# Kernel tuning notes

Measured on AMD Instinct MI355X. Metric: run time of the kernel, lower is better.

The kernel has to match this reference:

```python
import jax, jax.numpy as jnp
import numpy as np

B, S, D = 4, 2048, 512
H, HD, RL = 8, 64, 64   # nheads, head_dim = D//H, rl_dim
TEMPER = 1.0
BETA = 1.0
SLOPE = 0.01  # LeakyReLU negative slope
LN_EPS = 1e-5


def setup_inputs() -> dict:
    key = jax.random.key(0)
    ks = jax.random.split(key, 12)
    scale = 0.02
    return {
        "h":   jax.random.normal(ks[0], (B, S, D), dtype=jnp.float32),
        "rh":  jax.random.normal(ks[1], (B, S, RL), dtype=jnp.float32),
        "Wl":  jax.random.normal(ks[2], (D, D), dtype=jnp.float32) * scale,   # linear_l (in,out)
        "Wr":  jax.random.normal(ks[3], (D, D), dtype=jnp.float32) * scale,   # linear_r
        "al":  jax.random.normal(ks[4], (HD,), dtype=jnp.float32) * scale,    # att_l: Linear(head_dim,1)
        "ar":  jax.random.normal(ks[5], (HD,), dtype=jnp.float32) * scale,    # att_r
        "Wrs": jax.random.normal(ks[6], (RL, RL * H), dtype=jnp.float32) * scale,  # r_source
        "Wrt": jax.random.normal(ks[7], (RL, RL * H), dtype=jnp.float32) * scale,  # r_target
        "Wf":  jax.random.normal(ks[8], (D, D), dtype=jnp.float32) * scale,   # linear_final
        "ln_g": jnp.ones((D,), dtype=jnp.float32),
        "ln_b": jnp.zeros((D,), dtype=jnp.float32),
    }


def _layer_norm(x, g, b):
    mu = jnp.mean(x, axis=-1, keepdims=True)
    var = jnp.mean(jnp.square(x - mu), axis=-1, keepdims=True)
    return (x - mu) * jax.lax.rsqrt(var + LN_EPS) * g + b


def reference(h, rh, Wl, Wr, al, ar, Wrs, Wrt, Wf, ln_g, ln_b):
    leaky = lambda x: jnp.where(x >= 0, x, SLOPE * x)
    # projections -> [B, H, S, HD]
    fl = (h @ Wl).reshape(B, S, H, HD).transpose(0, 2, 1, 3)
    fr = (h @ Wr).reshape(B, S, H, HD).transpose(0, 2, 1, 3)
    # additive attention logits: [B,H,S,1] + [B,H,1,S]
    sl = jnp.einsum('bhsd,d->bhs', leaky(fl), al)
    sr = jnp.einsum('bhsd,d->bhs', leaky(fr), ar)
    score = sl[:, :, :, None] + sr[:, :, None, :]
    # relation-embedding bilinear bias: r_k @ r_q -> [B,H,S,S]
    r_k = (rh @ Wrs).reshape(B, S, H, RL).transpose(0, 2, 1, 3)   # [B,H,S,RL]
    r_q = (rh @ Wrt).reshape(B, S, H, RL).transpose(0, 2, 3, 1)   # [B,H,RL,S]
    score = score + BETA * jnp.einsum('bhsr,bhrt->bhst', r_k, r_q)
    score = jax.nn.softmax(score / TEMPER, axis=-1)
    # context and output projection (dropout = 0 -> identity)
    context = jnp.einsum('bhst,bhtd->bhsd', score, fr)
    h_sa = context.transpose(0, 2, 1, 3).reshape(B, S, H * HD)
    fh = h_sa @ Wf
    return _layer_norm(h + fh, ln_g, ln_b)
```

## Files before the change

### kernel.cpp

```cpp
#include <hip/hip_runtime.h>
#include <math.h>

#define B_ 4
#define S_ 2048
#define D_ 512
#define H_ 8
#define HD_ 64
#define RL_ 64
#define LN_EPS 1e-5f
#define SLOPE 0.01f
#define LOG2E 1.4426950408889634f

typedef __attribute__((ext_vector_type(8))) __bf16 bf16x8;
typedef __attribute__((ext_vector_type(4))) float f32x4;
typedef __attribute__((ext_vector_type(16))) float f32x16;

__device__ __forceinline__ float leaky(float x) { return x >= 0.f ? x : SLOPE * x; }

__device__ __forceinline__ ushort f2bf(float f) {
    union { float f; unsigned u; } v; v.f = f;
    unsigned r = v.u + 0x7fffu + ((v.u >> 16) & 1u);
    return (ushort)(r >> 16);
}
__device__ __forceinline__ unsigned cvtpk(float a, float b) {
    unsigned r;
    asm("v_cvt_pk_bf16_f32 %0, %1, %2" : "=v"(r) : "v"(a), "v"(b));
    return r;
}

__device__ __forceinline__ void g2lds16(const void* g, void* l) {
    __builtin_amdgcn_global_load_lds(
        (const __attribute__((address_space(1))) void*)(uintptr_t)g,
        (__attribute__((address_space(3))) void*)(uintptr_t)l, 16, 0, 0);
}

__device__ __forceinline__ void plane32swap(unsigned &x, unsigned &y) {
    asm volatile("v_permlane32_swap_b32 %0, %1" : "+v"(x), "+v"(y));
}

__global__ __launch_bounds__(256) void prep(
    const float* __restrict__ h, const float* __restrict__ rh,
    const float* __restrict__ Wr, const float* __restrict__ Wf,
    const float* __restrict__ Wrs, const float* __restrict__ Wrt,
    ushort* __restrict__ hb, ushort* __restrict__ rhb,
    ushort* __restrict__ WrT, ushort* __restrict__ WfT,
    ushort* __restrict__ WrsT, ushort* __restrict__ WrtT)
{
    const int bx = blockIdx.x, tid = threadIdx.x;
    if (bx < 4608) {
        const float* in = (bx < 4096) ? h : rh;
        ushort* o = (bx < 4096) ? hb : rhb;
        const int i = (bx < 4096 ? bx : bx - 4096) * 256 + tid;
        const float4 v = ((const float4*)in)[i];
        ushort4 u; u.x = f2bf(v.x); u.y = f2bf(v.y); u.z = f2bf(v.z); u.w = f2bf(v.w);
        ((ushort4*)o)[i] = u;
        return;
    }
    __shared__ float TS[64][65];
    int t = bx - 4608;
    const float* in; ushort* out; int K, tk, tn;
    if (t < 64)       { in = Wr;  out = WrT;  K = 512; tk = t & 7; tn = t >> 3; }
    else if (t < 128) { in = Wf;  out = WfT;  K = 512; t -= 64; tk = t & 7; tn = t >> 3; }
    else if (t < 136) { in = Wrs; out = WrsT; K = 64;  tk = 0; tn = t - 128; }
    else              { in = Wrt; out = WrtT; K = 64;  tk = 0; tn = t - 136; }
    const int k0 = tk * 64, n0 = tn * 64;
    const int r = tid >> 4, c4 = (tid & 15) * 4;
    #pragma unroll
    for (int p = 0; p < 4; ++p) {
        const int row = r + 16 * p;
        const float4 v = *(const float4*)(in + (size_t)(k0 + row) * 512 + n0 + c4);
        TS[row][c4] = v.x; TS[row][c4 + 1] = v.y;
        TS[row][c4 + 2] = v.z; TS[row][c4 + 3] = v.w;
    }
    __syncthreads();
    #pragma unroll
    for (int p = 0; p < 4; ++p) {
        const int nn = r + 16 * p;
        ushort4 o;
        o.x = f2bf(TS[c4 + 0][nn]); o.y = f2bf(TS[c4 + 1][nn]);
        o.z = f2bf(TS[c4 + 2][nn]); o.w = f2bf(TS[c4 + 3][nn]);
        *(ushort4*)(out + (size_t)(n0 + nn) * K + k0 + c4) = o;
    }
}

__global__ __launch_bounds__(256) void proj(
    const ushort* __restrict__ hb, const ushort* __restrict__ rhb,
    const ushort* __restrict__ WrT, const ushort* __restrict__ WrsT,
    const ushort* __restrict__ WrtT,
    ushort* __restrict__ frT, ushort* __restrict__ rkw, ushort* __restrict__ rqw,
    float* __restrict__ sred, const float* __restrict__ ar)
{
    __shared__ ushort As[2][64 * 32];
    __shared__ ushort Bs[2][128 * 32];

    const int tid = threadIdx.x;
    const int lane = tid & 63, w = tid >> 6;
    const int ln = lane & 15, quad = lane >> 4;
    const int wm = w >> 1, wn = w & 1;
    const int m0 = blockIdx.x * 64, n0 = blockIdx.y * 128;
    const int z = blockIdx.z;

    const ushort* A; const ushort* wt; ushort* co; float scl; int K;
    if (z == 0)      { A = hb;  wt = WrT;  co = frT; scl = LOG2E; K = 512; }
    else if (z == 1) { A = rhb; wt = WrsT; co = rkw; scl = LOG2E; K = 64; }
    else             { A = rhb; wt = WrtT; co = rqw; scl = 1.0f;  K = 64; }

    const int srA = tid >> 2;
    const int lchA = ((lane & 3) - (srA >> 1)) & 3;
    const ushort* AgB = A + (size_t)(m0 + srA) * K + lchA * 8;
    const int srB = w * 32 + (lane >> 2);
    const int lchB = ((lane & 3) - (srB >> 1)) & 3;
    const ushort* BgB0 = wt + (size_t)(n0 + srB) * K + lchB * 8;
    const ushort* BgB1 = BgB0 + (size_t)16 * K;
    const int aoff = tid * 8;
    const int boff = srB * 32 + (lane & 3) * 8;
    const int pc = (quad + (ln >> 1)) & 3;

    g2lds16(AgB, &As[0][aoff]);
    g2lds16(BgB0, &Bs[0][boff]);
    g2lds16(BgB1, &Bs[0][boff + 512]);

    f32x4 acc[2][4] = {};
    int buf = 0;
    for (int k0 = 0; k0 < K; k0 += 32) {
        __syncthreads();
        if (k0 + 32 < K) {
            g2lds16(AgB + k0 + 32, &As[buf ^ 1][aoff]);
            g2lds16(BgB0 + k0 + 32, &Bs[buf ^ 1][boff]);
            g2lds16(BgB1 + k0 + 32, &Bs[buf ^ 1][boff + 512]);
        }
        bf16x8 af[2], bfr[4];
        #pragma unroll
        for (int mi = 0; mi < 2; ++mi)
            af[mi] = *(const bf16x8*)&As[buf][(wm * 32 + mi * 16 + ln) * 32 + pc * 8];
        #pragma unroll
        for (int ni = 0; ni < 4; ++ni)
            bfr[ni] = *(const bf16x8*)&Bs[buf][(wn * 64 + ni * 16 + ln) * 32 + pc * 8];
        #pragma unroll
        for (int mi = 0; mi < 2; ++mi)
            #pragma unroll
            for (int ni = 0; ni < 4; ++ni)
                acc[mi][ni] = __builtin_amdgcn_mfma_f32_16x16x32_bf16(
                    af[mi], bfr[ni], acc[mi][ni], 0, 0, 0);
        buf ^= 1;
    }

    const int head = blockIdx.y * 2 + wn;
    const int b = m0 >> 11;
    const size_t bh = (size_t)b * H_ + head;
    if (z == 0) {
        #pragma unroll
        for (int mi = 0; mi < 2; ++mi) {
            const int s = (m0 & (S_ - 1)) + wm * 32 + mi * 16 + quad * 4;
            const int sp = (s & ~15) | ((((0x1320u >> (quad * 4)) & 0xFu)) << 2);
            #pragma unroll
            for (int ni = 0; ni < 4; ++ni) {
                const int d = ni * 16 + ln;
                ushort4 o;
                o.x = f2bf(acc[mi][ni][0]); o.y = f2bf(acc[mi][ni][1]);
                o.z = f2bf(acc[mi][ni][2]); o.w = f2bf(acc[mi][ni][3]);
                *(ushort4*)(co + (bh * 64 + d) * S_ + sp) = o;
            }
        }
        float a4[4];
        #pragma unroll
        for (int ni = 0; ni < 4; ++ni) a4[ni] = ar[ni * 16 + ln];
        #pragma unroll
        for (int mi = 0; mi < 2; ++mi) {
            const int s = (m0 & (S_ - 1)) + wm * 32 + mi * 16 + quad * 4;
            #pragma unroll
            for (int r = 0; r < 4; ++r) {
                float v = 0.f;
                #pragma unroll
                for (int ni = 0; ni < 4; ++ni)
                    v += leaky(acc[mi][ni][r]) * a4[ni];
                #pragma unroll
                for (int off = 8; off; off >>= 1) v += __shfl_xor(v, off, 16);
                if (ln == 0) sred[bh * S_ + s + r] = v * scl;
            }
        }
    } else {
        #pragma unroll
        for (int mi = 0; mi < 2; ++mi) {
            const int s = (m0 & (S_ - 1)) + wm * 32 + mi * 16 + quad * 4;
            #pragma unroll
            for (int ni = 0; ni < 4; ++ni) {
                const int d = ni * 16 + ln;
                #pragma unroll
                for (int r = 0; r < 4; ++r)
                    co[(bh * S_ + s + r) * 64 + d] = f2bf(acc[mi][ni][r] * scl);
            }
        }
    }
}

#define WAITV(N) asm volatile("s_waitcnt vmcnt(" #N ")" ::: "memory")
#define BARR()   __builtin_amdgcn_s_barrier()

__global__ __launch_bounds__(256, 1) void attn_mfma(
    const ushort* __restrict__ frT, const ushort* __restrict__ rk,
    const ushort* __restrict__ rq, const float* __restrict__ sr,
    ushort* __restrict__ hsa)
{
    __shared__ ushort SMEM[16384];
    __shared__ float  LS[4][2][64];
    ushort* RQp = SMEM;
    ushort* FTp = SMEM + 8192;

    const int tid = threadIdx.x;
    const int w = tid >> 6;
    const int qg = w >> 1;
    const int th = w & 1;
    const int lane = tid & 63;
    const int lq = lane & 31;
    const int hi = lane >> 5;

    const int flat = blockIdx.x + 16 * (blockIdx.y + 8 * blockIdx.z);
    const int wid = (flat & 7) * 64 + (flat >> 3);
    const int q0 = (wid & 15) * 128;
    const int h = (wid >> 4) & 7;
    const int b = wid >> 7;
    const size_t bh = (size_t)b * H_ + h;
    const int qb = q0 + 64 * qg;

    bf16x8 bq[2][4];
    #pragma unroll
    for (int qt = 0; qt < 2; ++qt) {
        const ushort* p = rk + ((bh * S_ + qb + 32 * qt + lq) << 6) + hi * 8;
        #pragma unroll
        for (int ks = 0; ks < 4; ++ks)
            bq[qt][ks] = *(const bf16x8*)(p + ks * 16);
    }

    const ushort* rq_g = rq + (bh * S_ << 6);
    const ushort* ft_g = frT + (size_t)bh * 64 * S_;
    const float* srp = sr + bh * S_;

    const int srow = tid >> 3;
    const int pg = tid & 7;
    const int oS = (pg - (srow & 7)) & 7;

    #define STAGE(BUF, t0)                                                    \
        { _Pragma("unroll")                                                   \
          for (int j = 0; j < 2; ++j) {                                       \
            const int rr = 32 * j + srow;                                     \
            g2lds16(rq_g + ((size_t)((t0) + rr) << 6) + oS * 8,               \
                    RQp + (BUF) * 4096 + rr * 64 + pg * 8);                   \
            g2lds16(ft_g + (size_t)rr * S_ + (t0) + oS * 8,                   \
                    FTp + (BUF) * 4096 + rr * 64 + pg * 8);                   \
          } }

    f32x16 ctx[2][2] = {};
    float lsum[2] = {0.f, 0.f};

    #define COMPUTE(BI, TC)                                                    \
    {                                                                          \
        bf16x8 af[4];                                                          \
        _Pragma("unroll")                                                      \
        for (int ks = 0; ks < 4; ++ks)                                         \
            af[ks] = *(const bf16x8*)(RQp + (BI) * 4096 + (th * 32 + lq) * 64  \
                       + ((2 * ks + hi + (lq & 7)) & 7) * 8);                  \
        f32x16 s0 = {}; f32x16 s1 = {};                                        \
        _Pragma("unroll")                                                      \
        for (int ks = 0; ks < 4; ++ks) {                                       \
            s0 = __builtin_amdgcn_mfma_f32_32x32x16_bf16(af[ks], bq[0][ks], s0, 0, 0, 0); \
            s1 = __builtin_amdgcn_mfma_f32_32x32x16_bf16(af[ks], bq[1][ks], s1, 0, 0, 0); \
        }                                                                      \
        float sva[16];                                                         \
        _Pragma("unroll")                                                      \
        for (int jj = 0; jj < 4; ++jj) {                                       \
            const float4 v = *(const float4*)(srp + (TC) + th * 32 + jj * 8 + hi * 4); \
            sva[jj * 4 + 0] = v.x; sva[jj * 4 + 1] = v.y;                      \
            sva[jj * 4 + 2] = v.z; sva[jj * 4 + 3] = v.w;                      \
        }                                                                      \
        uint4 paw[2][2];                                                       \
        _Pragma("unroll")                                                      \
        for (int qt = 0; qt < 2; ++qt) {                                       \
            float p[16];                                                       \
            _Pragma("unroll")                                                  \
            for (int r = 0; r < 16; ++r)                                       \
                p[r] = __builtin_amdgcn_exp2f((qt ? s1[r] : s0[r]) + sva[r]);  \
            float ls = 0.f;                                                    \
            _Pragma("unroll")                                                  \
            for (int r = 0; r < 16; ++r) ls += p[r];                           \
            lsum[qt] += ls;                                                    \
            _Pragma("unroll")                                                  \
            for (int c = 0; c < 2; ++c) {                                      \
                const int e = 8 * c;                                           \
                unsigned c01 = cvtpk(p[e + 0], p[e + 1]);                      \
                unsigned c23 = cvtpk(p[e + 2], p[e + 3]);                      \
                unsigned c45 = cvtpk(p[e + 4], p[e + 5]);                      \
                unsigned c67 = cvtpk(p[e + 6], p[e + 7]);                      \
                plane32swap(c45, c67);                                         \
                paw[qt][c] = make_uint4(c01, c23, c67, c45);                   \
            }                                                                  \
        }                                                                      \
        _Pragma("unroll")                                                      \
        for (int c = 0; c < 2; ++c) {                                          \
            _Pragma("unroll")                                                  \
            for (int dt = 0; dt < 2; ++dt) {                                   \
                const bf16x8 fv = *(const bf16x8*)(FTp + (BI) * 4096           \
                    + (dt * 32 + lq) * 64                                      \
                    + ((4 * th + 2 * c + hi + (lq & 7)) & 7) * 8);             \
                ctx[0][dt] = __builtin_amdgcn_mfma_f32_32x32x16_bf16(          \
                    __builtin_bit_cast(bf16x8, paw[0][c]), fv, ctx[0][dt], 0, 0, 0); \
                ctx[1][dt] = __builtin_amdgcn_mfma_f32_32x32x16_bf16(          \
                    __builtin_bit_cast(bf16x8, paw[1][c]), fv, ctx[1][dt], 0, 0, 0); \
            }                                                                  \
        }                                                                      \
    }

    STAGE(0, 0)
    for (int it = 0; it < 15; ++it) {
        const int t0 = it * 128;
        WAITV(0); BARR();
        STAGE(1, t0 + 64)
        COMPUTE(0, t0)
        WAITV(0); BARR();
        STAGE(0, t0 + 128)
        COMPUTE(1, t0 + 64)
    }
    WAITV(0); BARR();
    STAGE(1, 1984)
    COMPUTE(0, 1920)
    WAITV(0); BARR();
    COMPUTE(1, 1984)

    BARR();
    float* CX = (float*)SMEM;
    float* CXw = CX + w * 2048;

    #define EPILOGUE(OWN, OTH)                                                \
    {                                                                         \
        _Pragma("unroll")                                                     \
        for (int qt = 0; qt < 2; ++qt)                                        \
            _Pragma("unroll")                                                 \
            for (int r = 0; r < 16; ++r)                                      \
                CXw[(qt * 16 + r) * 64 + lane] = ctx[qt][OTH][r];             \
        LS[w][0][lane] = lsum[0];                                             \
        LS[w][1][lane] = lsum[1];                                             \
        BARR();                                                               \
        const float* CXp = CX + (w ^ 1) * 2048;                               \
        _Pragma("unroll")                                                     \
        for (int qt = 0; qt < 2; ++qt) {                                      \
            float lt = lsum[qt] + LS[w ^ 1][qt][lane];                        \
            const float l = lt + __shfl_xor(lt, 32, 64);                      \
            const float inv = 1.f / l;                                        \
            _Pragma("unroll")                                                 \
            for (int r = 0; r < 16; ++r) {                                    \
                const float cv = ctx[qt][OWN][r] + CXp[(qt * 16 + r) * 64 + lane]; \
                const int rho = (r & 3) + 8 * (r >> 2) + 4 * hi;              \
                const float fi = __shfl(inv, rho, 64);                        \
                const int q = qb + 32 * qt + rho;                             \
                hsa[(size_t)(b * S_ + q) * D_ + h * 64 + (OWN) * 32 + lq] = f2bf(cv * fi); \
            }                                                                 \
        }                                                                     \
    }

    if (th == 0) EPILOGUE(0, 1)
    else         EPILOGUE(1, 0)
}

__global__ __launch_bounds__(256, 1) void gemm_ln(
    const ushort* __restrict__ A, const ushort* __restrict__ WT,
    const float* __restrict__ hres, const float* __restrict__ g,
    const float* __restrict__ bb, float* __restrict__ out)
{
    __shared__ ushort As[2][32 * 32];
    __shared__ ushort Bs[2][512 * 32];
    __shared__ float  RS[32][4];

    const int tid = threadIdx.x;
    const int lane = tid & 63, w = tid >> 6;
    const int ln = lane & 15, quad = lane >> 4;
    const int K = 512;

    const int blk = (blockIdx.x & 7) * 32 + (blockIdx.x >> 3);
    const int m0 = blk * 32;

    const int srA = tid >> 2;
    const int lchA = ((lane & 3) - (srA >> 1)) & 3;
    const ushort* AgB = A + (size_t)(m0 + srA) * K + lchA * 8;
    const int aoff = tid * 8;

    const int rb = 128 * w + (lane >> 2);

    f32x4 acc[2][8] = {};

    if (tid < 128) g2lds16(AgB, &As[0][aoff]);
    #pragma unroll
    for (int j = 0; j < 8; ++j) {
        const int rw = rb + 16 * j;
        const int lchB = ((lane & 3) - (rw >> 1)) & 3;
        g2lds16(WT + (size_t)rw * K + lchB * 8, &Bs[0][rw * 32 + (lane & 3) * 8]);
    }

    const int pc = (quad + (ln >> 1)) & 3;
    int buf = 0;
    for (int k0 = 0; k0 < K; k0 += 32) {
        __syncthreads();
        if (k0 + 32 < K) {
            if (tid < 128) g2lds16(AgB + k0 + 32, &As[buf ^ 1][aoff]);
            #pragma unroll
            for (int j = 0; j < 8; ++j) {
                const int rw = rb + 16 * j;
                const int lchB = ((lane & 3) - (rw >> 1)) & 3;
                g2lds16(WT + (size_t)rw * K + k0 + 32 + lchB * 8,
                        &Bs[buf ^ 1][rw * 32 + (lane & 3) * 8]);
            }
        }
        bf16x8 af[2], bfr[8];
        #pragma unroll
        for (int mi = 0; mi < 2; ++mi)
            af[mi] = *(const bf16x8*)&As[buf][(mi * 16 + ln) * 32 + pc * 8];
        #pragma unroll
        for (int ni = 0; ni < 8; ++ni)
            bfr[ni] = *(const bf16x8*)&Bs[buf][(w * 128 + ni * 16 + ln) * 32 + pc * 8];
        #pragma unroll
        for (int mi = 0; mi < 2; ++mi)
            #pragma unroll
            for (int ni = 0; ni < 8; ++ni)
                acc[mi][ni] = __builtin_amdgcn_mfma_f32_16x16x32_bf16(
                    af[mi], bfr[ni], acc[mi][ni], 0, 0, 0);
        buf ^= 1;
    }

    float gg[8], bv[8];
    #pragma unroll
    for (int ni = 0; ni < 8; ++ni) {
        const int col = 128 * w + ni * 16 + ln;
        gg[ni] = g[col]; bv[ni] = bb[col];
    }

    #pragma unroll
    for (int mi = 0; mi < 2; ++mi)
        #pragma unroll
        for (int r = 0; r < 4; ++r) {
            const int rl = mi * 16 + quad * 4 + r;
            const float* hp = hres + (size_t)(m0 + rl) * 512 + 128 * w + ln;
            float s = 0.f;
            #pragma unroll
            for (int ni = 0; ni < 8; ++ni) {
                acc[mi][ni][r] += hp[ni * 16];
                s += acc[mi][ni][r];
            }
            #pragma unroll
            for (int off = 8; off; off >>= 1) s += __shfl_xor(s, off, 16);
            if (ln == 0) RS[rl][w] = s;
        }
    __syncthreads();
    float mu[2][4];
    #pragma unroll
    for (int mi = 0; mi < 2; ++mi)
        #pragma unroll
        for (int r = 0; r < 4; ++r) {
            const int rl = mi * 16 + quad * 4 + r;
            mu[mi][r] = (RS[rl][0] + RS[rl][1] + RS[rl][2] + RS[rl][3]) * (1.f / 512.f);
        }
    __syncthreads();
    #pragma unroll
    for (int mi = 0; mi < 2; ++mi)
        #pragma unroll
        for (int r = 0; r < 4; ++r) {
            const int rl = mi * 16 + quad * 4 + r;
            float v = 0.f;
            #pragma unroll
            for (int ni = 0; ni < 8; ++ni) {
                const float d = acc[mi][ni][r] - mu[mi][r];
                v += d * d;
            }
            #pragma unroll
            for (int off = 8; off; off >>= 1) v += __shfl_xor(v, off, 16);
            if (ln == 0) RS[rl][w] = v;
        }
    __syncthreads();
    #pragma unroll
    for (int mi = 0; mi < 2; ++mi)
        #pragma unroll
        for (int r = 0; r < 4; ++r) {
            const int rl = mi * 16 + quad * 4 + r;
            const float var = (RS[rl][0] + RS[rl][1] + RS[rl][2] + RS[rl][3]) * (1.f / 512.f);
            const float inv = rsqrtf(var + LN_EPS);
            float* op = out + (size_t)(m0 + rl) * 512 + 128 * w + ln;
            #pragma unroll
            for (int ni = 0; ni < 8; ++ni)
                op[ni * 16] = (acc[mi][ni][r] - mu[mi][r]) * inv * gg[ni] + bv[ni];
        }
}

extern "C" void kernel_launch(void* const* d_in, const int* in_sizes, int n_in,
                              void* d_out, int out_size, void* d_ws, size_t ws_size,
                              hipStream_t stream)
{
    const float* h   = (const float*)d_in[0];
    const float* rh  = (const float*)d_in[1];
    const float* Wr  = (const float*)d_in[3];
    const float* ar  = (const float*)d_in[5];
    const float* Wrs = (const float*)d_in[6];
    const float* Wrt = (const float*)d_in[7];
    const float* Wf  = (const float*)d_in[8];
    const float* lng = (const float*)d_in[9];
    const float* lnb = (const float*)d_in[10];
    float* out = (float*)d_out;
    char* wsb  = (char*)d_ws;

    const size_t MB = (size_t)1 << 20;
    ushort* hb   = (ushort*)(wsb);
    ushort* rhb  = (ushort*)(wsb + 8 * MB);
    ushort* WrT  = (ushort*)(wsb + 9 * MB);
    ushort* WfT  = (ushort*)(wsb + 9 * MB + 512 * 1024);
    ushort* WrsT = (ushort*)(wsb + 10 * MB);
    ushort* WrtT = (ushort*)(wsb + 10 * MB + 64 * 1024);
    ushort* frT  = (ushort*)(wsb + 11 * MB);
    ushort* rkw  = (ushort*)(wsb + 19 * MB);
    ushort* rqw  = (ushort*)(wsb + 27 * MB);
    float*  sr   = (float*) (wsb + 35 * MB);
    ushort* hsab = (ushort*)(wsb + 36 * MB);

    dim3 blk(256);
    prep<<<dim3(4752), blk, 0, stream>>>(h, rh, Wr, Wf, Wrs, Wrt,
                                         hb, rhb, WrT, WfT, WrsT, WrtT);
    proj<<<dim3(128, 4, 3), blk, 0, stream>>>(hb, rhb, WrT, WrsT, WrtT,
                                              frT, rkw, rqw, sr, ar);
    attn_mfma<<<dim3(S_ / 128, H_, B_), blk, 0, stream>>>(frT, rkw, rqw, sr, hsab);
    gemm_ln<<<dim3(256), blk, 0, stream>>>(hsab, WfT, h, lng, lnb, out);
}
```

Measured before the change: 177.7 us.

## Stage proj outputs through LDS for coalesced stores; halve gemm_ln row tile

The proj kernel's non-score branch now writes its bf16 results into shared memory first, then stores them back to global memory as contiguous 16-byte rows instead of scattered 2-byte writes. The final GEMM+LayerNorm kernel drops from 32-row to 16-row tiles and launches 512 blocks instead of 256, so more CUs have work on the 256-CU-class device. In exchange, each gemm_ln block reads the full Wf tile for half as many rows, which doubles weight traffic. The projection epilogue also gains extra barriers.

```diff
diff --git a/kernel.cpp b/kernel.cpp
--- a/kernel.cpp
+++ b/kernel.cpp
@@ -180,16 +180,33 @@
             }
         }
     } else {
+        __syncthreads();
+        ushort* TMP = &Bs[0][0];
         #pragma unroll
         for (int mi = 0; mi < 2; ++mi) {
-            const int s = (m0 & (S_ - 1)) + wm * 32 + mi * 16 + quad * 4;
+            const int sl = wm * 32 + mi * 16 + quad * 4;
             #pragma unroll
             for (int ni = 0; ni < 4; ++ni) {
-                const int d = ni * 16 + ln;
+                const int c = wn * 64 + ni * 16 + ln;
                 #pragma unroll
                 for (int r = 0; r < 4; ++r)
-                    co[(bh * S_ + s + r) * 64 + d] = f2bf(acc[mi][ni][r] * scl);
+                    TMP[(sl + r) * 128 + c] = f2bf(acc[mi][ni][r] * scl);
             }
+        }
+        __syncthreads();
+        const int rr = tid >> 4;
+        const int cc = (tid & 15) * 8;
+        const int hh = cc >> 6;
+        const size_t bhb = (size_t)b * H_ + blockIdx.y * 2 + hh;
+        #pragma unroll
+        for (int p = 0; p < 4; ++p) {
+            const int row = rr + 16 * p;
+            const int s = (m0 & (S_ - 1)) + row;
+            const ushort4 v0 = *(const ushort4*)&TMP[row * 128 + cc];
+            const ushort4 v1 = *(const ushort4*)&TMP[row * 128 + cc + 4];
+            ushort* dst = co + (bhb * S_ + s) * 64 + (cc & 63);
+            *(ushort4*)dst = v0;
+            *(ushort4*)(dst + 4) = v1;
         }
     }
 }
@@ -366,17 +383,17 @@
     const float* __restrict__ hres, const float* __restrict__ g,
     const float* __restrict__ bb, float* __restrict__ out)
 {
-    __shared__ ushort As[2][32 * 32];
+    __shared__ ushort As[2][16 * 32];
     __shared__ ushort Bs[2][512 * 32];
-    __shared__ float  RS[32][4];
+    __shared__ float  RS[16][4];
 
     const int tid = threadIdx.x;
     const int lane = tid & 63, w = tid >> 6;
     const int ln = lane & 15, quad = lane >> 4;
     const int K = 512;
 
-    const int blk = (blockIdx.x & 7) * 32 + (blockIdx.x >> 3);
-    const int m0 = blk * 32;
+    const int blk = (blockIdx.x & 7) * 64 + (blockIdx.x >> 3);
+    const int m0 = blk * 16;
 
     const int srA = tid >> 2;
     const int lchA = ((lane & 3) - (srA >> 1)) & 3;
@@ -385,9 +402,9 @@
 
     const int rb = 128 * w + (lane >> 2);
 
-    f32x4 acc[2][8] = {};
-
-    if (tid < 128) g2lds16(AgB, &As[0][aoff]);
+    f32x4 acc[8] = {};
+
+    if (tid < 64) g2lds16(AgB, &As[0][aoff]);
     #pragma unroll
     for (int j = 0; j < 8; ++j) {
         const int rw = rb + 16 * j;
@@ -400,7 +417,7 @@
     for (int k0 = 0; k0 < K; k0 += 32) {
         __syncthreads();
         if (k0 + 32 < K) {
-            if (tid < 128) g2lds16(AgB + k0 + 32, &As[buf ^ 1][aoff]);
+            if (tid < 64) g2lds16(AgB + k0 + 32, &As[buf ^ 1][aoff]);
             #pragma unroll
             for (int j = 0; j < 8; ++j) {
                 const int rw = rb + 16 * j;
@@ -409,19 +426,14 @@
                         &Bs[buf ^ 1][rw * 32 + (lane & 3) * 8]);
             }
         }
-        bf16x8 af[2], bfr[8];
-        #pragma unroll
-        for (int mi = 0; mi < 2; ++mi)
-            af[mi] = *(const bf16x8*)&As[buf][(mi * 16 + ln) * 32 + pc * 8];
+        const bf16x8 af = *(const bf16x8*)&As[buf][ln * 32 + pc * 8];
+        bf16x8 bfr[8];
         #pragma unroll
         for (int ni = 0; ni < 8; ++ni)
             bfr[ni] = *(const bf16x8*)&Bs[buf][(w * 128 + ni * 16 + ln) * 32 + pc * 8];
         #pragma unroll
-        for (int mi = 0; mi < 2; ++mi)
-            #pragma unroll
-            for (int ni = 0; ni < 8; ++ni)
-                acc[mi][ni] = __builtin_amdgcn_mfma_f32_16x16x32_bf16(
-                    af[mi], bfr[ni], acc[mi][ni], 0, 0, 0);
+        for (int ni = 0; ni < 8; ++ni)
+            acc[ni] = __builtin_amdgcn_mfma_f32_16x16x32_bf16(af, bfr[ni], acc[ni], 0, 0, 0);
         buf ^= 1;
     }
 
@@ -433,59 +445,51 @@
     }
 
     #pragma unroll
-    for (int mi = 0; mi < 2; ++mi)
-        #pragma unroll
-        for (int r = 0; r < 4; ++r) {
-            const int rl = mi * 16 + quad * 4 + r;
-            const float* hp = hres + (size_t)(m0 + rl) * 512 + 128 * w + ln;
-            float s = 0.f;
-            #pragma unroll
-            for (int ni = 0; ni < 8; ++ni) {
-                acc[mi][ni][r] += hp[ni * 16];
-                s += acc[mi][ni][r];
-            }
-            #pragma unroll
-            for (int off = 8; off; off >>= 1) s += __shfl_xor(s, off, 16);
-            if (ln == 0) RS[rl][w] = s;
-        }
+    for (int r = 0; r < 4; ++r) {
+        const int rl = quad * 4 + r;
+        const float* hp = hres + (size_t)(m0 + rl) * 512 + 128 * w + ln;
+        float s = 0.f;
+        #pragma unroll
+        for (int ni = 0; ni < 8; ++ni) {
+            acc[ni][r] += hp[ni * 16];
+            s += acc[ni][r];
+        }
+        #pragma unroll
+        for (int off = 8; off; off >>= 1) s += __shfl_xor(s, off, 16);
+        if (ln == 0) RS[rl][w] = s;
+    }
     __syncthreads();
-    float mu[2][4];
-    #pragma unroll
-    for (int mi = 0; mi < 2; ++mi)
-        #pragma unroll
-        for (int r = 0; r < 4; ++r) {
-            const int rl = mi * 16 + quad * 4 + r;
-            mu[mi][r] = (RS[rl][0] + RS[rl][1] + RS[rl][2] + RS[rl][3]) * (1.f / 512.f);
-        }
+    float mu[4];
+    #pragma unroll
+    for (int r = 0; r < 4; ++r) {
+        const int rl = quad * 4 + r;
+        mu[r] = (RS[rl][0] + RS[rl][1] + RS[rl][2] + RS[rl][3]) * (1.f / 512.f);
+    }
     __syncthreads();
     #pragma unroll
-    for (int mi = 0; mi < 2; ++mi)
-        #pragma unroll
-        for (int r = 0; r < 4; ++r) {
-            const int rl = mi * 16 + quad * 4 + r;
-            float v = 0.f;
-            #pragma unroll
-            for (int ni = 0; ni < 8; ++ni) {
-                const float d = acc[mi][ni][r] - mu[mi][r];
-                v += d * d;
-            }
-            #pragma unroll
-            for (int off = 8; off; off >>= 1) v += __shfl_xor(v, off, 16);
-            if (ln == 0) RS[rl][w] = v;
-        }
+    for (int r = 0; r < 4; ++r) {
+        const int rl = quad * 4 + r;
+        float v = 0.f;
+        #pragma unroll
+        for (int ni = 0; ni < 8; ++ni) {
+            const float d = acc[ni][r] - mu[r];
+            v += d * d;
+        }
+        #pragma unroll
+        for (int off = 8; off; off >>= 1) v += __shfl_xor(v, off, 16);
+        if (ln == 0) RS[rl][w] = v;
+    }
     __syncthreads();
     #pragma unroll
-    for (int mi = 0; mi < 2; ++mi)
-        #pragma unroll
-        for (int r = 0; r < 4; ++r) {
-            const int rl = mi * 16 + quad * 4 + r;
-            const float var = (RS[rl][0] + RS[rl][1] + RS[rl][2] + RS[rl][3]) * (1.f / 512.f);
-            const float inv = rsqrtf(var + LN_EPS);
-            float* op = out + (size_t)(m0 + rl) * 512 + 128 * w + ln;
-            #pragma unroll
-            for (int ni = 0; ni < 8; ++ni)
-                op[ni * 16] = (acc[mi][ni][r] - mu[mi][r]) * inv * gg[ni] + bv[ni];
-        }
+    for (int r = 0; r < 4; ++r) {
+        const int rl = quad * 4 + r;
+        const float var = (RS[rl][0] + RS[rl][1] + RS[rl][2] + RS[rl][3]) * (1.f / 512.f);
+        const float inv = rsqrtf(var + LN_EPS);
+        float* op = out + (size_t)(m0 + rl) * 512 + 128 * w + ln;
+        #pragma unroll
+        for (int ni = 0; ni < 8; ++ni)
+            op[ni * 16] = (acc[ni][r] - mu[r]) * inv * gg[ni] + bv[ni];
+    }
 }
 
 extern "C" void kernel_launch(void* const* d_in, const int* in_sizes, int n_in,
@@ -523,5 +527,5 @@
     proj<<<dim3(128, 4, 3), blk, 0, stream>>>(hb, rhb, WrT, WrsT, WrtT,
                                               frT, rkw, rqw, sr, ar);
     attn_mfma<<<dim3(S_ / 128, H_, B_), blk, 0, stream>>>(frT, rkw, rqw, sr, hsab);
-    gemm_ln<<<dim3(256), blk, 0, stream>>>(hsab, WfT, h, lng, lnb, out);
-}
+    gemm_ln<<<dim3(512), blk, 0, stream>>>(hsab, WfT, h, lng, lnb, out);
+}
```

New measurement: 178.7 us. No clear change (+0.6%).
